# Kernel tuning notes

Measured on AMD Instinct MI355X. Metric: run time of the kernel, lower is better.

Reference implementation:

```python
import jax, jax.numpy as jnp
import numpy as np
from jax import lax

B, L = 4, 2048
D_MODEL, D_STATE, D_CONV, EXPAND = 1024, 16, 4, 2
D_INNER = EXPAND * D_MODEL          # 2048
DT_RANK = (D_MODEL + 15) // 16      # 64 (mamba_ssm 'auto')
EPS = 1e-5


def setup_inputs() -> dict:
    key = jax.random.key(0)
    ks = jax.random.split(key, 10)
    s = 0.02
    x = jax.random.normal(ks[0], (B, L, D_MODEL), dtype=jnp.float32)
    ln_w = jnp.ones((D_MODEL,), jnp.float32)
    ln_b = jnp.zeros((D_MODEL,), jnp.float32)
    W_in = jax.random.normal(ks[1], (2 * D_INNER, D_MODEL), jnp.float32) * s
    conv_w = jax.random.normal(ks[2], (D_INNER, 1, D_CONV), jnp.float32) * s
    conv_b = jnp.zeros((D_INNER,), jnp.float32)
    W_x = jax.random.normal(ks[3], (DT_RANK + 2 * D_STATE, D_INNER), jnp.float32) * s
    W_dt = jax.random.normal(ks[4], (D_INNER, DT_RANK), jnp.float32) * s
    b_dt = jax.random.uniform(ks[5], (D_INNER,), jnp.float32, -4.0, -2.0)  # softplus(b)~small dt
    A_log = jnp.log(jnp.tile(jnp.arange(1.0, D_STATE + 1.0, dtype=jnp.float32), (D_INNER, 1)))
    Dp = jnp.ones((D_INNER,), jnp.float32)
    W_out = jax.random.normal(ks[6], (D_MODEL, D_INNER), jnp.float32) * s
    return dict(x=x, ln_w=ln_w, ln_b=ln_b, W_in=W_in, conv_w=conv_w, conv_b=conv_b,
                W_x=W_x, W_dt=W_dt, b_dt=b_dt, A_log=A_log, Dp=Dp, W_out=W_out)


def _mamba_forward(x, ln_w, ln_b, W_in, conv_w, conv_b, W_x, W_dt, b_dt, A_log, Dp, W_out):
    # LayerNorm
    mu = jnp.mean(x, axis=-1, keepdims=True)
    var = jnp.mean(jnp.square(x - mu), axis=-1, keepdims=True)
    xn = (x - mu) * lax.rsqrt(var + EPS) * ln_w + ln_b

    # in_proj -> (x_in, z), each [B, L, D_INNER]
    xz = jnp.einsum('bld,ed->ble', xn, W_in)
    x_in, z = jnp.split(xz, 2, axis=-1)

    # depthwise causal conv1d over time + SiLU
    xt = jnp.transpose(x_in, (0, 2, 1))  # [B, D_INNER, L]
    xc = lax.conv_general_dilated(xt, conv_w, window_strides=(1,),
                                  padding=[(D_CONV - 1, 0)],
                                  feature_group_count=D_INNER)
    xc = jax.nn.silu(jnp.transpose(xc + conv_b[None, :, None], (0, 2, 1)))  # [B, L, D_INNER]

    # SSM parameterization
    x_dbl = jnp.einsum('bld,ed->ble', xc, W_x)  # [B, L, DT_RANK + 2*D_STATE]
    dt_r, Bs, Cs = jnp.split(x_dbl, [DT_RANK, DT_RANK + D_STATE], axis=-1)
    dt = jax.nn.softplus(jnp.einsum('blr,dr->bld', dt_r, W_dt) + b_dt)  # [B, L, D_INNER]
    A = -jnp.exp(A_log)  # [D_INNER, D_STATE]

    # selective scan over time (time-major)
    def step(h, inp):
        dt_t, B_t, C_t, u_t = inp  # [B,dI], [B,dS], [B,dS], [B,dI]
        dA = jnp.exp(dt_t[:, :, None] * A)                     # [B, dI, dS]
        h = dA * h + (dt_t * u_t)[:, :, None] * B_t[:, None, :]
        y = jnp.sum(h * C_t[:, None, :], axis=-1)              # [B, dI]
        return h, y

    h0 = jnp.zeros((B, D_INNER, D_STATE), x.dtype)
    xs = (jnp.swapaxes(dt, 0, 1), jnp.swapaxes(Bs, 0, 1),
          jnp.swapaxes(Cs, 0, 1), jnp.swapaxes(xc, 0, 1))
    _, ys = lax.scan(step, h0, xs)
    y = jnp.swapaxes(ys, 0, 1) + xc * Dp  # [B, L, D_INNER]

    # gate + out_proj + residual
    y = y * jax.nn.silu(z)
    out = jnp.einsum('ble,de->bld', y, W_out)
    return x + out


def reference(x, ln_w, ln_b, W_in, conv_w, conv_b, W_x, W_dt, b_dt, A_log, Dp, W_out):
    return _mamba_forward(x, ln_w, ln_b, W_in, conv_w, conv_b, W_x, W_dt, b_dt, A_log, Dp, W_out)
```

## Files before the change

kernel.cpp:

```cpp
#include <hip/hip_runtime.h>
#include <math.h>

#define BB 4
#define LL 2048
#define DM 1024
#define DI 2048
#define DS 16
#define DTR 64
#define TCH 256
#define TT 16

typedef unsigned short bf16;
typedef __attribute__((ext_vector_type(8))) short bf16x8;
typedef __attribute__((ext_vector_type(4))) float f32x4;

__device__ inline float b2f(bf16 u) { return __uint_as_float(((unsigned)u) << 16); }
__device__ inline bf16 f2b(float f) {
    unsigned u = __float_as_uint(f);
    u += 0x7FFF + ((u >> 16) & 1);
    return (bf16)(u >> 16);
}

__device__ inline float4 ld4(const float* p) { return *(const float4*)p; }
__device__ inline float4 ld4(const bf16* p) {
    ushort4 v = *(const ushort4*)p;
    return make_float4(b2f(v.x), b2f(v.y), b2f(v.z), b2f(v.w));
}
__device__ inline void st1(float* p, float v) { *p = v; }
__device__ inline void st1(bf16* p, float v) { *p = f2b(v); }

__device__ inline float softplus_fast(float v) {
    return (v > 15.f) ? v : __logf(1.f + __expf(v));
}

__device__ inline void gld_lds16(const void* g, void* l) {
    __builtin_amdgcn_global_load_lds(
        (const __attribute__((address_space(1))) unsigned int*)g,
        (__attribute__((address_space(3))) unsigned int*)l, 16, 0, 0);
}

__global__ __launch_bounds__(256) void f2b_kernel(const float* __restrict__ in,
    bf16* __restrict__ out, int n4)
{
    int i = blockIdx.x * 256 + threadIdx.x;
    if (i >= n4) return;
    float4 v = *(const float4*)(in + (size_t)i * 4);
    ushort4 o = { f2b(v.x), f2b(v.y), f2b(v.z), f2b(v.w) };
    *(ushort4*)(out + (size_t)i * 4) = o;
}

__global__ __launch_bounds__(256) void convw_transpose(
    const float* __restrict__ cw, bf16* __restrict__ cwt)
{
    int d = blockIdx.x * 256 + threadIdx.x;
    if (d >= DI) return;
    float4 w = *(const float4*)(cw + d * 4);
    cwt[0 * DI + d] = f2b(w.x);
    cwt[1 * DI + d] = f2b(w.y);
    cwt[2 * DI + d] = f2b(w.z);
    cwt[3 * DI + d] = f2b(w.w);
}

__global__ void af_init(int* f) { if (threadIdx.x == 0) *f = 0; }

__global__ __launch_bounds__(256) void af_check(const float* __restrict__ A, int* f)
{
    int g = blockIdx.x * 256 + threadIdx.x;
    int d = g >> 4, s = g & 15;
    float a0 = __expf(A[(size_t)d * DS]);
    float as = __expf(A[g]);
    float tgt = (float)(s + 1) * a0;
    if (fabsf(as - tgt) > 1e-5f * fabsf(tgt) + 1e-30f) atomicOr(f, 1);
}

__global__ __launch_bounds__(256) void ln_kernel(const float* __restrict__ x,
    const float* __restrict__ w, const float* __restrict__ b,
    bf16* __restrict__ xn)
{
    int row = blockIdx.x;
    int tid = threadIdx.x;
    const float* xr = x + (size_t)row * DM;
    float4 v = *(const float4*)(xr + tid * 4);
    float s1 = v.x + v.y + v.z + v.w;
    float s2 = v.x * v.x + v.y * v.y + v.z * v.z + v.w * v.w;
    #pragma unroll
    for (int o = 32; o > 0; o >>= 1) {
        s1 += __shfl_xor(s1, o);
        s2 += __shfl_xor(s2, o);
    }
    __shared__ float r1[4], r2[4];
    __shared__ float smu, srs;
    int wv = tid >> 6;
    if ((tid & 63) == 0) { r1[wv] = s1; r2[wv] = s2; }
    __syncthreads();
    if (tid == 0) {
        float t1 = r1[0] + r1[1] + r1[2] + r1[3];
        float t2 = r2[0] + r2[1] + r2[2] + r2[3];
        float mu = t1 * (1.0f / DM);
        float var = t2 * (1.0f / DM) - mu * mu;
        smu = mu;
        srs = rsqrtf(var + 1e-5f);
    }
    __syncthreads();
    float mu = smu, rs = srs;
    float4 wv4 = *(const float4*)(w + tid * 4);
    float4 bv4 = *(const float4*)(b + tid * 4);
    ushort4 o;
    o.x = f2b((v.x - mu) * rs * wv4.x + bv4.x);
    o.y = f2b((v.y - mu) * rs * wv4.y + bv4.y);
    o.z = f2b((v.z - mu) * rs * wv4.z + bv4.z);
    o.w = f2b((v.w - mu) * rs * wv4.w + bv4.w);
    *(ushort4*)(xn + (size_t)row * DM + tid * 4) = o;
}

#define BARR  do { asm volatile("" ::: "memory"); __builtin_amdgcn_s_barrier(); \
                   asm volatile("" ::: "memory"); } while (0)
#define LGKM0 do { asm volatile("s_waitcnt lgkmcnt(0)" ::: "memory"); \
                   __builtin_amdgcn_sched_barrier(0); } while (0)
#define VMC4  asm volatile("s_waitcnt vmcnt(4)" ::: "memory")

template<int EPI, typename TC>
__global__ __launch_bounds__(512, 2) void gemm_8p(
    const bf16* __restrict__ A, int lda,
    const bf16* __restrict__ B, int ldb,
    TC* __restrict__ C, int ldc,
    int K, const float* __restrict__ aux, int nbn)
{
    __shared__ bf16 lds[65536];
    char* L = (char*)lds;
    const int tid = threadIdx.x;
    const int lane = tid & 63;
    const int w = tid >> 6;
    const int wm = w >> 2;
    const int wn = w & 3;

    int nwg = gridDim.x;
    int bid = blockIdx.x;
    int sb = bid;
    if ((nwg & 7) == 0) sb = (bid & 7) * (nwg >> 3) + (bid >> 3);
    const int m0 = (sb / nbn) * 256;
    const int n0 = (sb % nbn) * 256;

    const size_t lda2 = (size_t)lda * 2;
    const size_t ldb2 = (size_t)ldb * 2;
    const int l8 = lane >> 3;
    const int scol = ((lane & 7) ^ l8) << 4;
    const size_t offA = (size_t)(w * 8 + l8) * lda2 + scol;
    const size_t offB = (size_t)(w * 8 + l8) * ldb2 + scol;
    const char* Ab = (const char*)A + (size_t)m0 * lda2;
    const char* Bb = (const char*)B + (size_t)n0 * ldb2;

    const int fm = lane & 15, fq = lane >> 4;
    const int prow = fm * 128;
    const int px0 = (fq << 4) ^ ((fm & 7) << 4);
    const int px1 = (64 | (fq << 4)) ^ ((fm & 7) << 4);
    const char* Lar = L + wm * 16384 + prow;
    const char* Lbr = L + 65536 + (wn >> 1) * 16384 + (wn & 1) * 8192 + prow;

    f32x4 acc[8][4] = {};
    bf16x8 a_[2][2], b_[4][2];

#define ST_A(sbuf, hh, t) do { \
    const char* s_ = Ab + (size_t)(hh) * 128 * lda2 + (size_t)(t) * 128 + offA; \
    gld_lds16(s_,             L + (sbuf) * 32768 + (hh) * 16384 + w * 1024); \
    gld_lds16(s_ + 64 * lda2, L + (sbuf) * 32768 + (hh) * 16384 + 8192 + w * 1024); \
  } while (0)
#define ST_B(sbuf, hh, t) do { \
    const char* s_ = Bb + (size_t)(hh) * 128 * ldb2 + (size_t)(t) * 128 + offB; \
    gld_lds16(s_,             L + 65536 + (sbuf) * 32768 + (hh) * 16384 + w * 1024); \
    gld_lds16(s_ + 64 * ldb2, L + 65536 + (sbuf) * 32768 + (hh) * 16384 + 8192 + w * 1024); \
  } while (0)
#define DS_A(rb, q) do { \
    a_[0][0] = *(const bf16x8*)(Lar + (rb) * 32768 + ((q) * 32 +  0) * 128 + px0); \
    a_[0][1] = *(const bf16x8*)(Lar + (rb) * 32768 + ((q) * 32 +  0) * 128 + px1); \
    a_[1][0] = *(const bf16x8*)(Lar + (rb) * 32768 + ((q) * 32 + 16) * 128 + px0); \
    a_[1][1] = *(const bf16x8*)(Lar + (rb) * 32768 + ((q) * 32 + 16) * 128 + px1); \
  } while (0)
#define DS_B(rb) do { \
    _Pragma("unroll") \
    for (int ni = 0; ni < 4; ni++) { \
      b_[ni][0] = *(const bf16x8*)(Lbr + (rb) * 32768 + ni * 2048 + px0); \
      b_[ni][1] = *(const bf16x8*)(Lbr + (rb) * 32768 + ni * 2048 + px1); \
    } } while (0)
#define MFMA_Q(q) do { \
    __builtin_amdgcn_s_setprio(1); \
    _Pragma("unroll") \
    for (int mi = 0; mi < 2; mi++) \
      _Pragma("unroll") \
      for (int ni = 0; ni < 4; ni++) { \
        acc[(q)*2+mi][ni] = __builtin_amdgcn_mfma_f32_16x16x32_bf16( \
            a_[mi][0], b_[ni][0], acc[(q)*2+mi][ni], 0, 0, 0); \
        acc[(q)*2+mi][ni] = __builtin_amdgcn_mfma_f32_16x16x32_bf16( \
            a_[mi][1], b_[ni][1], acc[(q)*2+mi][ni], 0, 0, 0); \
      } \
    __builtin_amdgcn_s_setprio(0); \
  } while (0)

    const int NT = K >> 6;
    ST_B(0, 0, 0); ST_B(0, 1, 0);
    ST_A(0, 0, 0); ST_A(0, 1, 0);
    ST_B(1, 0, 1); ST_B(1, 1, 1);
    VMC4;
    BARR;

    for (int t0 = 0; t0 < NT; t0 += 2) {
        const int tA1 = t0 + 1;
        const int tN2 = (t0 + 2 < NT) ? t0 + 2 : NT - 1;
        const int tN3 = (t0 + 3 < NT) ? t0 + 3 : NT - 1;
        DS_A(0, 0); DS_B(0); ST_A(1, 0, tA1);
        BARR; LGKM0; MFMA_Q(0); BARR;
        DS_A(0, 1); ST_A(1, 1, tA1);
        BARR; LGKM0; MFMA_Q(1); BARR;
        DS_A(0, 2); ST_B(0, 0, tN2);
        BARR; LGKM0; MFMA_Q(2); BARR;
        DS_A(0, 3); ST_B(0, 1, tN2);
        VMC4;
        BARR; LGKM0; MFMA_Q(3); BARR;
        DS_A(1, 0); DS_B(1); ST_A(0, 0, tN2);
        BARR; LGKM0; MFMA_Q(0); BARR;
        DS_A(1, 1); ST_A(0, 1, tN2);
        BARR; LGKM0; MFMA_Q(1); BARR;
        DS_A(1, 2); ST_B(1, 0, tN3);
        BARR; LGKM0; MFMA_Q(2); BARR;
        DS_A(1, 3); ST_B(1, 1, tN3);
        VMC4;
        BARR; LGKM0; MFMA_Q(3); BARR;
    }
    asm volatile("s_waitcnt vmcnt(0)" ::: "memory");

    #pragma unroll
    for (int i = 0; i < 8; i++) {
        #pragma unroll
        for (int ni = 0; ni < 4; ni++) {
            int n = n0 + wn * 64 + ni * 16 + fm;
            #pragma unroll
            for (int r = 0; r < 4; r++) {
                int m = m0 + wm * 128 + i * 16 + fq * 4 + r;
                float v = acc[i][ni][r];
                if (EPI == 2) v += aux[(size_t)m * ldc + n];
                st1(&C[(size_t)m * ldc + n], v);
            }
        }
    }
#undef ST_A
#undef ST_B
#undef DS_A
#undef DS_B
#undef MFMA_Q
}

template<int EPI, typename TC>
__global__ __launch_bounds__(256) void gemm_mfma(
    const bf16* __restrict__ A, int lda,
    const bf16* __restrict__ B, int ldb,
    TC* __restrict__ C, int ldc,
    int K, const float* __restrict__ aux)
{
    __shared__ bf16 As[128 * 32];
    __shared__ bf16 Bs[128 * 32];
    const int tid = threadIdx.x;
    const int lane = tid & 63;
    const int w = tid >> 6;
    const int wm = w >> 1, wn = w & 1;
    const int m0 = blockIdx.y * 128, n0 = blockIdx.x * 128;

    const int srow = lane >> 2;
    const int schunk = (lane & 3) * 8;

    const int fm = lane & 15;
    const int fq = lane >> 4;

    f32x4 acc[4][4] = {};

    for (int kt = 0; kt < K; kt += 32) {
        #pragma unroll
        for (int i = 0; i < 2; i++) {
            int r0 = i * 64 + w * 16;
            gld_lds16(A + (size_t)(m0 + r0 + srow) * lda + kt + schunk, &As[r0 * 32]);
            gld_lds16(B + (size_t)(n0 + r0 + srow) * ldb + kt + schunk, &Bs[r0 * 32]);
        }
        __syncthreads();
        bf16x8 af[4], bfr[4];
        #pragma unroll
        for (int i = 0; i < 4; i++) {
            af[i]  = *(const bf16x8*)&As[(wm * 64 + i * 16 + fm) * 32 + fq * 8];
            bfr[i] = *(const bf16x8*)&Bs[(wn * 64 + i * 16 + fm) * 32 + fq * 8];
        }
        #pragma unroll
        for (int i = 0; i < 4; i++)
            #pragma unroll
            for (int j = 0; j < 4; j++)
                acc[i][j] = __builtin_amdgcn_mfma_f32_16x16x32_bf16(
                    af[i], bfr[j], acc[i][j], 0, 0, 0);
        __syncthreads();
    }

    #pragma unroll
    for (int i = 0; i < 4; i++) {
        #pragma unroll
        for (int r = 0; r < 4; r++) {
            int m = m0 + wm * 64 + i * 16 + fq * 4 + r;
            #pragma unroll
            for (int j = 0; j < 4; j++) {
                int n = n0 + wn * 64 + j * 16 + fm;
                float v = acc[i][j][r];
                if (EPI == 1) {
                    v = softplus_fast(v + aux[n]);
                } else if (EPI == 2) {
                    v += aux[(size_t)m * ldc + n];
                }
                st1(&C[(size_t)m * ldc + n], v);
            }
        }
    }
}

__global__ __launch_bounds__(256) void xproj_mfma(
    const bf16* __restrict__ A,
    const bf16* __restrict__ Bm,
    float* __restrict__ Cx,
    bf16* __restrict__ dtr)
{
    __shared__ bf16 As[32 * 32];
    __shared__ bf16 Bs[128 * 32];
    const int tid = threadIdx.x;
    const int lane = tid & 63;
    const int w = tid >> 6;
    const int wm = w >> 1, wn = w & 1;
    const int m0 = blockIdx.x * 32;
    const int srow = lane >> 2;
    const int schunk = (lane & 3) * 8;
    const int fm = lane & 15;
    const int fq = lane >> 4;
    f32x4 acc[3] = {};
    for (int kt = 0; kt < DI; kt += 32) {
        if (w < 2) {
            int r0 = w * 16;
            gld_lds16(A + (size_t)(m0 + r0 + srow) * DI + kt + schunk, &As[r0 * 32]);
        }
        {
            int r0 = w * 32;
            gld_lds16(Bm + (size_t)(r0 + srow) * DI + kt + schunk, &Bs[r0 * 32]);
            gld_lds16(Bm + (size_t)(r0 + 16 + srow) * DI + kt + schunk, &Bs[(r0 + 16) * 32]);
        }
        __syncthreads();
        bf16x8 af = *(const bf16x8*)&As[(wm * 16 + fm) * 32 + fq * 8];
        #pragma unroll
        for (int j = 0; j < 3; j++) {
            bf16x8 bf = *(const bf16x8*)&Bs[((wn * 3 + j) * 16 + fm) * 32 + fq * 8];
            acc[j] = __builtin_amdgcn_mfma_f32_16x16x32_bf16(af, bf, acc[j], 0, 0, 0);
        }
        __syncthreads();
    }
    #pragma unroll
    for (int j = 0; j < 3; j++) {
        int col = (wn * 3 + j) * 16 + fm;
        #pragma unroll
        for (int r = 0; r < 4; r++) {
            int m = m0 + wm * 16 + fq * 4 + r;
            float v = acc[j][r];
            Cx[(size_t)m * 96 + col] = v;
            if (col < 64) dtr[(size_t)m * 64 + col] = f2b(v);
        }
    }
}

template<int EPI, typename TA, typename TB, typename TC>
__global__ __launch_bounds__(256) void gemm_nt(
    const TA* __restrict__ A, int lda,
    const TB* __restrict__ B, int ldb,
    TC* __restrict__ C, int ldc,
    int M, int N, int K,
    const float* __restrict__ aux)
{
    __shared__ float As[16][64];
    __shared__ float Bs[16][64];
    int tid = threadIdx.x;
    int m0 = blockIdx.y * 64, n0 = blockIdx.x * 64;
    int lr = tid >> 2;
    int lc = (tid & 3) * 4;
    int tm = tid >> 4;
    int tn = tid & 15;
    float acc[4][4] = {};
    for (int kt = 0; kt < K; kt += 16) {
        float4 av = ld4(A + (size_t)(m0 + lr) * lda + kt + lc);
        float4 bv = make_float4(0.f, 0.f, 0.f, 0.f);
        if (n0 + lr < N)
            bv = ld4(B + (size_t)(n0 + lr) * ldb + kt + lc);
        As[lc + 0][lr] = av.x; As[lc + 1][lr] = av.y;
        As[lc + 2][lr] = av.z; As[lc + 3][lr] = av.w;
        Bs[lc + 0][lr] = bv.x; Bs[lc + 1][lr] = bv.y;
        Bs[lc + 2][lr] = bv.z; Bs[lc + 3][lr] = bv.w;
        __syncthreads();
        #pragma unroll
        for (int k = 0; k < 16; k++) {
            float4 a4 = *(const float4*)&As[k][tm * 4];
            float4 b4 = *(const float4*)&Bs[k][tn * 4];
            float am[4] = {a4.x, a4.y, a4.z, a4.w};
            float bn[4] = {b4.x, b4.y, b4.z, b4.w};
            #pragma unroll
            for (int i = 0; i < 4; i++)
                #pragma unroll
                for (int j = 0; j < 4; j++)
                    acc[i][j] = fmaf(am[i], bn[j], acc[i][j]);
        }
        __syncthreads();
    }
    #pragma unroll
    for (int i = 0; i < 4; i++) {
        int m = m0 + tm * 4 + i;
        #pragma unroll
        for (int j = 0; j < 4; j++) {
            int n = n0 + tn * 4 + j;
            if (n >= N) continue;
            float v = acc[i][j];
            if (EPI == 1) {
                v = softplus_fast(v + aux[n]);
            }
            st1(&C[(size_t)m * ldc + n], v);
        }
    }
}

__global__ __launch_bounds__(256) void conv_silu_kernel(
    const bf16* __restrict__ xz, const bf16* __restrict__ cwt,
    const float* __restrict__ cb, bf16* __restrict__ xc)
{
    int idx = blockIdx.x * 256 + threadIdx.x;
    int d8 = idx & (DI / 8 - 1);
    int bl = idx >> 8;
    int l = bl & (LL - 1);
    int d0 = d8 * 8;
    float4 b0 = *(const float4*)(cb + d0);
    float4 b1 = *(const float4*)(cb + d0 + 4);
    float acc[8] = {b0.x, b0.y, b0.z, b0.w, b1.x, b1.y, b1.z, b1.w};
    #pragma unroll
    for (int k = 0; k < 4; k++) {
        if (l - 3 + k < 0) continue;
        bf16x8 xv = *(const bf16x8*)(xz + (size_t)(bl - 3 + k) * (2 * DI) + d0);
        bf16x8 wv = *(const bf16x8*)(cwt + k * DI + d0);
        #pragma unroll
        for (int j = 0; j < 8; j++)
            acc[j] = fmaf(b2f((bf16)xv[j]), b2f((bf16)wv[j]), acc[j]);
    }
    bf16x8 o;
    #pragma unroll
    for (int j = 0; j < 8; j++)
        o[j] = (short)f2b(acc[j] / (1.f + __expf(-acc[j])));
    *(bf16x8*)(xc + (size_t)bl * DI + d0) = o;
}

template<int NCC>
__global__ __launch_bounds__(256) void scan_part1(
    const float* __restrict__ xdbl, const bf16* __restrict__ dty,
    const bf16* __restrict__ xc, const float* __restrict__ A_log,
    float* __restrict__ P, float* __restrict__ S, const int* __restrict__ aflag)
{
    __shared__ bf16 sdt[TT][TCH];
    __shared__ bf16 su[TT][TCH];
    __shared__ alignas(16) float sBC[TT][32];
    const int CH = LL / NCC;
    int bid = blockIdx.x;
    int cg = bid & 7;
    int c  = (bid >> 3) & (NCC - 1);
    int b  = (bid >> 3) / NCC;
    int d0 = cg * TCH;
    int tid = threadIdx.x;
    int w = tid >> 6, l = tid & 63;
    int lrow = l >> 5, lcol = (l & 31) * 8;
    int brow = l >> 3, bcol = (l & 7) * 4;
    int d = d0 + tid;

    const int structured = (__builtin_amdgcn_readfirstlane(aflag[0]) == 0);

    float Ads[16];
    #pragma unroll
    for (int q = 0; q < 4; q++) {
        float4 a4 = *(const float4*)&A_log[(size_t)d * DS + q * 4];
        Ads[q*4+0] = -__expf(a4.x); Ads[q*4+1] = -__expf(a4.y);
        Ads[q*4+2] = -__expf(a4.z); Ads[q*4+3] = -__expf(a4.w);
    }
    const float A0 = Ads[0];
    float h[16];
    #pragma unroll
    for (int s = 0; s < 16; s++) h[s] = 0.f;
    float dsum = 0.f;

    const size_t rowbase = (size_t)b * LL + c * CH;
    for (int t0 = 0; t0 < CH; t0 += TT) {
        #pragma unroll
        for (int pp = 0; pp < 2; pp++) {
            int r0 = (pp * 4 + w) * 2;
            size_t grow = rowbase + t0 + r0 + lrow;
            gld_lds16(dty + grow * DI + d0 + lcol, &sdt[r0][0]);
            gld_lds16(xc  + grow * DI + d0 + lcol, &su[r0][0]);
        }
        if (w < 2)
            gld_lds16(xdbl + (rowbase + t0 + w * 8 + brow) * 96 + DTR + bcol,
                      &sBC[w * 8][0]);
        __syncthreads();
        for (int t = 0; t < TT; t++) {
            float dtv = b2f(sdt[t][tid]);
            float uv  = b2f(su[t][tid]);
            float tmp = dtv * uv;
            dsum += dtv;
            const float4* bc = (const float4*)&sBC[t][0];
            float4 B0 = bc[0], B1 = bc[1], B2 = bc[2], B3 = bc[3];
            float Bv[16] = {B0.x,B0.y,B0.z,B0.w, B1.x,B1.y,B1.z,B1.w,
                            B2.x,B2.y,B2.z,B2.w, B3.x,B3.y,B3.z,B3.w};
            if (structured) {
                float e1 = __expf(dtv * A0);
                float dA = e1;
                #pragma unroll
                for (int s = 0; s < 16; s++) {
                    h[s] = dA * h[s] + tmp * Bv[s];
                    dA *= e1;
                }
            } else {
                #pragma unroll
                for (int s = 0; s < 16; s++) {
                    float dA = __expf(dtv * Ads[s]);
                    h[s] = dA * h[s] + tmp * Bv[s];
                }
            }
        }
        __syncthreads();
    }
    size_t o = ((size_t)(b * NCC + c) * DI + d) * DS;
    #pragma unroll
    for (int q = 0; q < 4; q++) {
        float4 pv = make_float4(__expf(Ads[q*4+0]*dsum), __expf(Ads[q*4+1]*dsum),
                                __expf(Ads[q*4+2]*dsum), __expf(Ads[q*4+3]*dsum));
        *(float4*)&P[o + q*4] = pv;
        *(float4*)&S[o + q*4] = make_float4(h[q*4], h[q*4+1], h[q*4+2], h[q*4+3]);
    }
}

template<int NCC>
__global__ __launch_bounds__(256) void scan_combine(
    const float* __restrict__ P, float* __restrict__ S)
{
    int g = blockIdx.x * 256 + threadIdx.x;
    int b = g >> 15;
    int rem = g & 32767;
    float h = 0.f;
    #pragma unroll
    for (int c = 0; c < NCC; c++) {
        size_t o = ((size_t)(b * NCC + c) << 15) + rem;
        float p = P[o], sv = S[o];
        S[o] = h;
        h = p * h + sv;
    }
}

template<int NCC>
__global__ __launch_bounds__(256) void scan_part2(
    const float* __restrict__ xdbl, bf16* __restrict__ dty,
    const bf16* __restrict__ xc, const bf16* __restrict__ xz,
    const float* __restrict__ A_log, const float* __restrict__ Dp,
    const float* __restrict__ Hin, const int* __restrict__ aflag)
{
    __shared__ bf16 sdt[TT][TCH];
    __shared__ bf16 su[TT][TCH];
    __shared__ bf16 sz[TT][TCH];
    __shared__ alignas(16) float sBC[TT][32];
    const int CH = LL / NCC;
    int bid = blockIdx.x;
    int cg = bid & 7;
    int c  = (bid >> 3) & (NCC - 1);
    int b  = (bid >> 3) / NCC;
    int d0 = cg * TCH;
    int tid = threadIdx.x;
    int w = tid >> 6, l = tid & 63;
    int lrow = l >> 5, lcol = (l & 31) * 8;
    int brow = l >> 3, bcol = (l & 7) * 4;
    int d = d0 + tid;

    const int structured = (__builtin_amdgcn_readfirstlane(aflag[0]) == 0);

    float Ads[16];
    #pragma unroll
    for (int q = 0; q < 4; q++) {
        float4 a4 = *(const float4*)&A_log[(size_t)d * DS + q * 4];
        Ads[q*4+0] = -__expf(a4.x); Ads[q*4+1] = -__expf(a4.y);
        Ads[q*4+2] = -__expf(a4.z); Ads[q*4+3] = -__expf(a4.w);
    }
    const float A0 = Ads[0];
    float h[16];
    size_t ho = ((size_t)(b * NCC + c) * DI + d) * DS;
    #pragma unroll
    for (int q = 0; q < 4; q++) {
        float4 hv = *(const float4*)&Hin[ho + q*4];
        h[q*4] = hv.x; h[q*4+1] = hv.y; h[q*4+2] = hv.z; h[q*4+3] = hv.w;
    }
    float dpd = Dp[d];

    const size_t rowbase = (size_t)b * LL + c * CH;
    for (int t0 = 0; t0 < CH; t0 += TT) {
        #pragma unroll
        for (int pp = 0; pp < 2; pp++) {
            int r0 = (pp * 4 + w) * 2;
            size_t grow = rowbase + t0 + r0 + lrow;
            gld_lds16(dty + grow * DI + d0 + lcol, &sdt[r0][0]);
            gld_lds16(xc  + grow * DI + d0 + lcol, &su[r0][0]);
            gld_lds16(xz  + grow * (2 * DI) + DI + d0 + lcol, &sz[r0][0]);
        }
        if (w < 2)
            gld_lds16(xdbl + (rowbase + t0 + w * 8 + brow) * 96 + DTR + bcol,
                      &sBC[w * 8][0]);
        __syncthreads();
        for (int t = 0; t < TT; t++) {
            float dtv = b2f(sdt[t][tid]);
            float uv  = b2f(su[t][tid]);
            float tmp = dtv * uv;
            const float4* bc = (const float4*)&sBC[t][0];
            float4 B0 = bc[0], B1 = bc[1], B2 = bc[2], B3 = bc[3];
            float4 C0 = bc[4], C1 = bc[5], C2 = bc[6], C3 = bc[7];
            float Bv[16] = {B0.x,B0.y,B0.z,B0.w, B1.x,B1.y,B1.z,B1.w,
                            B2.x,B2.y,B2.z,B2.w, B3.x,B3.y,B3.z,B3.w};
            float Cv[16] = {C0.x,C0.y,C0.z,C0.w, C1.x,C1.y,C1.z,C1.w,
                            C2.x,C2.y,C2.z,C2.w, C3.x,C3.y,C3.z,C3.w};
            float y0 = 0.f, y1 = 0.f;
            if (structured) {
                float e1 = __expf(dtv * A0);
                float dA = e1;
                #pragma unroll
                for (int s = 0; s < 16; s++) {
                    h[s] = dA * h[s] + tmp * Bv[s];
                    if (s & 1) y1 = fmaf(h[s], Cv[s], y1);
                    else       y0 = fmaf(h[s], Cv[s], y0);
                    dA *= e1;
                }
            } else {
                #pragma unroll
                for (int s = 0; s < 16; s++) {
                    float dA = __expf(dtv * Ads[s]);
                    h[s] = dA * h[s] + tmp * Bv[s];
                    if (s & 1) y1 = fmaf(h[s], Cv[s], y1);
                    else       y0 = fmaf(h[s], Cv[s], y0);
                }
            }
            float y = y0 + y1;
            float zv = b2f(sz[t][tid]);
            float yo = (y + uv * dpd) * (zv / (1.f + __expf(-zv)));
            dty[(rowbase + t0 + t) * DI + d] = f2b(yo);
        }
        __syncthreads();
    }
}

__global__ __launch_bounds__(256) void scan_mono(
    const float* __restrict__ xdbl, bf16* __restrict__ dty,
    const bf16* __restrict__ xc, const bf16* __restrict__ xz,
    const float* __restrict__ A_log, const float* __restrict__ Dp)
{
    const int TC = 64;
    int b = blockIdx.x >> 7;
    int dblk = blockIdx.x & 127;
    int d0 = dblk * 16;
    int tid = threadIdx.x;
    int s = tid & 15;
    int dg = tid >> 4;
    int d = d0 + dg;
    float Ads = -__expf(A_log[(size_t)d * DS + s]);
    float h = 0.f;
    __shared__ float sdt[TC][16], su[TC][16], sB[TC][16], sC[TC][16], sy[TC][16];
    const size_t rowbase = (size_t)b * LL;
    int wi = tid >> 2;
    int wj = (tid & 3) * 4;
    float4 dpv = *(const float4*)(Dp + d0 + wj);
    for (int t0 = 0; t0 < LL; t0 += TC) {
        {
            size_t g = (rowbase + t0 + wi) * (size_t)DI + d0 + wj;
            *(float4*)&sdt[wi][wj] = ld4(dty + g);
            *(float4*)&su[wi][wj]  = ld4(xc + g);
        }
        #pragma unroll
        for (int r = 0; r < 4; r++) {
            int i = (tid >> 4) + r * 16;
            size_t g = (rowbase + t0 + i) * 96;
            sB[i][s] = xdbl[g + DTR + s];
            sC[i][s] = xdbl[g + DTR + DS + s];
        }
        __syncthreads();
        for (int i = 0; i < TC; i++) {
            float dtv = sdt[i][dg];
            float dA = __expf(dtv * Ads);
            h = dA * h + dtv * su[i][dg] * sB[i][s];
            float yp = h * sC[i][s];
            yp += __shfl_xor(yp, 1);
            yp += __shfl_xor(yp, 2);
            yp += __shfl_xor(yp, 4);
            yp += __shfl_xor(yp, 8);
            if (s == 0) sy[i][dg] = yp;
        }
        __syncthreads();
        {
            size_t g  = (rowbase + t0 + wi) * (size_t)DI + d0 + wj;
            size_t gz = (rowbase + t0 + wi) * (size_t)(2 * DI) + DI + d0 + wj;
            float4 zv = ld4(xz + gz);
            float4 yv = *(const float4*)&sy[wi][wj];
            float4 uv = *(const float4*)&su[wi][wj];
            ushort4 o;
            o.x = f2b((yv.x + uv.x * dpv.x) * (zv.x / (1.f + __expf(-zv.x))));
            o.y = f2b((yv.y + uv.y * dpv.y) * (zv.y / (1.f + __expf(-zv.y))));
            o.z = f2b((yv.z + uv.z * dpv.z) * (zv.z / (1.f + __expf(-zv.z))));
            o.w = f2b((yv.w + uv.w * dpv.w) * (zv.w / (1.f + __expf(-zv.w))));
            *(ushort4*)(dty + g) = o;
        }
        __syncthreads();
    }
}

__global__ __launch_bounds__(256) void conv_silu_slow(
    const bf16* __restrict__ xz, const float* __restrict__ cw,
    const float* __restrict__ cb, bf16* __restrict__ xc)
{
    int idx = blockIdx.x * 256 + threadIdx.x;
    int d4 = idx & (DI / 4 - 1);
    int bl = idx >> 9;
    int l = bl & (LL - 1);
    int d0 = d4 * 4;
    float4 bias = *(const float4*)(cb + d0);
    float acc[4] = {bias.x, bias.y, bias.z, bias.w};
    #pragma unroll
    for (int k = 0; k < 4; k++) {
        if (l - 3 + k < 0) continue;
        float4 xv = ld4(xz + (size_t)(bl - 3 + k) * (2 * DI) + d0);
        acc[0] = fmaf(xv.x, cw[(d0 + 0) * 4 + k], acc[0]);
        acc[1] = fmaf(xv.y, cw[(d0 + 1) * 4 + k], acc[1]);
        acc[2] = fmaf(xv.z, cw[(d0 + 2) * 4 + k], acc[2]);
        acc[3] = fmaf(xv.w, cw[(d0 + 3) * 4 + k], acc[3]);
    }
    ushort4 o;
    o.x = f2b(acc[0] / (1.f + __expf(-acc[0])));
    o.y = f2b(acc[1] / (1.f + __expf(-acc[1])));
    o.z = f2b(acc[2] / (1.f + __expf(-acc[2])));
    o.w = f2b(acc[3] / (1.f + __expf(-acc[3])));
    *(ushort4*)(xc + (size_t)bl * DI + d0) = o;
}

extern "C" void kernel_launch(void* const* d_in, const int* in_sizes, int n_in,
                              void* d_out, int out_size, void* d_ws, size_t ws_size,
                              hipStream_t stream)
{
    const float* x      = (const float*)d_in[0];
    const float* ln_w   = (const float*)d_in[1];
    const float* ln_b   = (const float*)d_in[2];
    const float* W_in   = (const float*)d_in[3];
    const float* conv_w = (const float*)d_in[4];
    const float* conv_b = (const float*)d_in[5];
    const float* W_x    = (const float*)d_in[6];
    const float* W_dt   = (const float*)d_in[7];
    const float* b_dt   = (const float*)d_in[8];
    const float* A_log  = (const float*)d_in[9];
    const float* Dp     = (const float*)d_in[10];
    const float* W_out  = (const float*)d_in[11];
    float* out = (float*)d_out;

    const size_t R = (size_t)BB * LL;

    bf16*  xz    = (bf16*)d_ws;
    bf16*  dty   = xz + R * 2 * DI;
    float* xdbl  = (float*)(dty + R * DI);
    float* Pbuf  = xdbl + R * 96;

    const size_t headB = (size_t)((char*)Pbuf - (char*)d_ws);
    const size_t tailB = (size_t)(128 * DI + DI * DTR + R * DTR + 4 * DI) * 2 + 64;
    const size_t ps32B = (size_t)BB * 32 * DI * DS * 4;
    const size_t ps16B = (size_t)BB * 16 * DI * DS * 4;
    const int ncc = (ws_size >= headB + 2 * ps32B + tailB) ? 32 : 16;
    const size_t psB = (ncc == 32) ? ps32B : ps16B;

    float* Sbuf   = (float*)((char*)Pbuf + psB);
    bf16*  W_x_b  = (bf16*)((char*)Sbuf + psB);
    bf16*  W_dt_b = W_x_b + 128 * DI;
    bf16*  dtr    = W_dt_b + DI * DTR;
    bf16*  cwt    = dtr + R * DTR;
    int*   aflag  = (int*)(cwt + 4 * DI);
    const size_t ws_need = (size_t)((char*)(aflag + 16) - (char*)d_ws);
    const bool fast = ws_size >= ws_need;

    bf16*  W_in_b  = dty;
    bf16*  W_out_b = xz;

    bf16* xn = (bf16*)d_out;
    bf16* xc = (bf16*)d_out;

    f2b_kernel<<<(2 * DI * DM / 4) / 256, 256, 0, stream>>>(W_in, W_in_b, 2 * DI * DM / 4);
    if (fast) {
        f2b_kernel<<<(96 * DI / 4 + 255) / 256, 256, 0, stream>>>(W_x, W_x_b, 96 * DI / 4);
        f2b_kernel<<<(DI * DTR / 4 + 255) / 256, 256, 0, stream>>>(W_dt, W_dt_b, DI * DTR / 4);
        convw_transpose<<<DI / 256, 256, 0, stream>>>(conv_w, cwt);
        af_init<<<1, 64, 0, stream>>>(aflag);
        af_check<<<DI * DS / 256, 256, 0, stream>>>(A_log, aflag);
    }

    ln_kernel<<<(int)R, 256, 0, stream>>>(x, ln_w, ln_b, xn);

    gemm_8p<0, bf16><<<dim3((int)(R / 256) * (2 * DI / 256)), 512, 0, stream>>>(
        xn, DM, W_in_b, DM, xz, 2 * DI, DM, nullptr, 2 * DI / 256);

    if (fast) {
        conv_silu_kernel<<<(int)(R * DI / 8 / 256), 256, 0, stream>>>(
            xz, cwt, conv_b, xc);
        xproj_mfma<<<(int)(R / 32), 256, 0, stream>>>(xc, W_x_b, xdbl, dtr);
        gemm_mfma<1, bf16><<<dim3(DI / 128, R / 128), 256, 0, stream>>>(
            dtr, DTR, W_dt_b, DTR, dty, DI, DTR, b_dt);
        if (ncc == 32) {
            scan_part1<32><<<BB * 32 * (DI / TCH), 256, 0, stream>>>(
                xdbl, dty, xc, A_log, Pbuf, Sbuf, aflag);
            scan_combine<32><<<BB * DI * DS / 256, 256, 0, stream>>>(Pbuf, Sbuf);
            scan_part2<32><<<BB * 32 * (DI / TCH), 256, 0, stream>>>(
                xdbl, dty, xc, xz, A_log, Dp, Sbuf, aflag);
        } else {
            scan_part1<16><<<BB * 16 * (DI / TCH), 256, 0, stream>>>(
                xdbl, dty, xc, A_log, Pbuf, Sbuf, aflag);
            scan_combine<16><<<BB * DI * DS / 256, 256, 0, stream>>>(Pbuf, Sbuf);
            scan_part2<16><<<BB * 16 * (DI / TCH), 256, 0, stream>>>(
                xdbl, dty, xc, xz, A_log, Dp, Sbuf, aflag);
        }
    } else {
        conv_silu_slow<<<(int)(R * DI / 4 / 256), 256, 0, stream>>>(
            xz, conv_w, conv_b, xc);
        gemm_nt<0><<<dim3(2, R / 64), 256, 0, stream>>>(
            xc, DI, W_x, DI, xdbl, 96, (int)R, 96, DI, nullptr);
        gemm_nt<1><<<dim3(DI / 64, R / 64), 256, 0, stream>>>(
            xdbl, 96, W_dt, DTR, dty, DI, (int)R, DI, DTR, b_dt);
        scan_mono<<<BB * (DI / 16), 256, 0, stream>>>(
            xdbl, dty, xc, xz, A_log, Dp);
    }

    f2b_kernel<<<(DM * DI / 4) / 256, 256, 0, stream>>>(W_out, W_out_b, DM * DI / 4);

    gemm_8p<2, float><<<dim3((int)(R / 256) * (DM / 256)), 512, 0, stream>>>(
        dty, DI, W_out_b, DI, out, DM, DI, x, DM / 256);
}
```

Measured before the change: 431.7 us.

## Software-pipeline LDS fragment reads with MFMA in the 8-phase GEMM

Splits each MFMA quarter into two k-halves. The LDS fragment loads for the next quarter (and next buffer's B fragments at quarter 3) are issued between and after those halves, so they overlap matrix work instead of stalling ahead of it. A prologue preloads the first fragments before the loop. This is meant to hide LDS read latency in the GEMM's main loop. It costs extra register pressure from live prefetched fragments, and it relies on barrier and waitcnt placement staying correct under the new read ordering.

```diff
diff --git a/kernel.cpp b/kernel.cpp
--- a/kernel.cpp
+++ b/kernel.cpp
@@ -118,6 +118,7 @@
 #define LGKM0 do { asm volatile("s_waitcnt lgkmcnt(0)" ::: "memory"); \
                    __builtin_amdgcn_sched_barrier(0); } while (0)
 #define VMC4  asm volatile("s_waitcnt vmcnt(4)" ::: "memory")
+#define SCHED0 __builtin_amdgcn_sched_barrier(0)
 
 template<int EPI, typename TC>
 __global__ __launch_bounds__(512, 2) void gemm_8p(
@@ -170,30 +171,39 @@
     gld_lds16(s_,             L + 65536 + (sbuf) * 32768 + (hh) * 16384 + w * 1024); \
     gld_lds16(s_ + 64 * ldb2, L + 65536 + (sbuf) * 32768 + (hh) * 16384 + 8192 + w * 1024); \
   } while (0)
-#define DS_A(rb, q) do { \
-    a_[0][0] = *(const bf16x8*)(Lar + (rb) * 32768 + ((q) * 32 +  0) * 128 + px0); \
-    a_[0][1] = *(const bf16x8*)(Lar + (rb) * 32768 + ((q) * 32 +  0) * 128 + px1); \
-    a_[1][0] = *(const bf16x8*)(Lar + (rb) * 32768 + ((q) * 32 + 16) * 128 + px0); \
-    a_[1][1] = *(const bf16x8*)(Lar + (rb) * 32768 + ((q) * 32 + 16) * 128 + px1); \
+#define DS_A1(rb, q, kh) do { \
+    a_[0][kh] = *(const bf16x8*)(Lar + (rb) * 32768 + ((q) * 32 +  0) * 128 + ((kh) ? px1 : px0)); \
+    a_[1][kh] = *(const bf16x8*)(Lar + (rb) * 32768 + ((q) * 32 + 16) * 128 + ((kh) ? px1 : px0)); \
   } while (0)
-#define DS_B(rb) do { \
+#define DS_Bh(rb, kh) do { \
     _Pragma("unroll") \
-    for (int ni = 0; ni < 4; ni++) { \
-      b_[ni][0] = *(const bf16x8*)(Lbr + (rb) * 32768 + ni * 2048 + px0); \
-      b_[ni][1] = *(const bf16x8*)(Lbr + (rb) * 32768 + ni * 2048 + px1); \
-    } } while (0)
-#define MFMA_Q(q) do { \
-    __builtin_amdgcn_s_setprio(1); \
+    for (int ni = 0; ni < 4; ni++) \
+      b_[ni][kh] = *(const bf16x8*)(Lbr + (rb) * 32768 + ni * 2048 + ((kh) ? px1 : px0)); \
+  } while (0)
+#define MFMA_H(q, kh) do { \
     _Pragma("unroll") \
     for (int mi = 0; mi < 2; mi++) \
       _Pragma("unroll") \
-      for (int ni = 0; ni < 4; ni++) { \
+      for (int ni = 0; ni < 4; ni++) \
         acc[(q)*2+mi][ni] = __builtin_amdgcn_mfma_f32_16x16x32_bf16( \
-            a_[mi][0], b_[ni][0], acc[(q)*2+mi][ni], 0, 0, 0); \
-        acc[(q)*2+mi][ni] = __builtin_amdgcn_mfma_f32_16x16x32_bf16( \
-            a_[mi][1], b_[ni][1], acc[(q)*2+mi][ni], 0, 0, 0); \
-      } \
+            a_[mi][kh], b_[ni][kh], acc[(q)*2+mi][ni], 0, 0, 0); \
+  } while (0)
+#define PHASE(rb, q, rb2, q2, STAGE, DOVMC) do { \
+    STAGE; \
+    if (DOVMC) VMC4; \
+    BARR; LGKM0; \
+    __builtin_amdgcn_s_setprio(1); \
+    MFMA_H(q, 0); \
     __builtin_amdgcn_s_setprio(0); \
+    DS_A1(rb2, q2, 0); \
+    if ((q) == 3) DS_Bh(rb2, 0); \
+    SCHED0; \
+    __builtin_amdgcn_s_setprio(1); \
+    MFMA_H(q, 1); \
+    __builtin_amdgcn_s_setprio(0); \
+    DS_A1(rb2, q2, 1); \
+    if ((q) == 3) DS_Bh(rb2, 1); \
+    BARR; \
   } while (0)
 
     const int NT = K >> 6;
@@ -202,29 +212,21 @@
     ST_B(1, 0, 1); ST_B(1, 1, 1);
     VMC4;
     BARR;
+    DS_Bh(0, 0); DS_Bh(0, 1);
+    DS_A1(0, 0, 0); DS_A1(0, 0, 1);
 
     for (int t0 = 0; t0 < NT; t0 += 2) {
         const int tA1 = t0 + 1;
         const int tN2 = (t0 + 2 < NT) ? t0 + 2 : NT - 1;
         const int tN3 = (t0 + 3 < NT) ? t0 + 3 : NT - 1;
-        DS_A(0, 0); DS_B(0); ST_A(1, 0, tA1);
-        BARR; LGKM0; MFMA_Q(0); BARR;
-        DS_A(0, 1); ST_A(1, 1, tA1);
-        BARR; LGKM0; MFMA_Q(1); BARR;
-        DS_A(0, 2); ST_B(0, 0, tN2);
-        BARR; LGKM0; MFMA_Q(2); BARR;
-        DS_A(0, 3); ST_B(0, 1, tN2);
-        VMC4;
-        BARR; LGKM0; MFMA_Q(3); BARR;
-        DS_A(1, 0); DS_B(1); ST_A(0, 0, tN2);
-        BARR; LGKM0; MFMA_Q(0); BARR;
-        DS_A(1, 1); ST_A(0, 1, tN2);
-        BARR; LGKM0; MFMA_Q(1); BARR;
-        DS_A(1, 2); ST_B(1, 0, tN3);
-        BARR; LGKM0; MFMA_Q(2); BARR;
-        DS_A(1, 3); ST_B(1, 1, tN3);
-        VMC4;
-        BARR; LGKM0; MFMA_Q(3); BARR;
+        PHASE(0, 0, 0, 1, ST_A(1, 0, tA1), 0);
+        PHASE(0, 1, 0, 2, ST_A(1, 1, tA1), 0);
+        PHASE(0, 2, 0, 3, ST_B(0, 0, tN2), 0);
+        PHASE(0, 3, 1, 0, ST_B(0, 1, tN2), 1);
+        PHASE(1, 0, 1, 1, ST_A(0, 0, tN2), 0);
+        PHASE(1, 1, 1, 2, ST_A(0, 1, tN2), 0);
+        PHASE(1, 2, 1, 3, ST_B(1, 0, tN3), 0);
+        PHASE(1, 3, 0, 0, ST_B(1, 1, tN3), 1);
     }
     asm volatile("s_waitcnt vmcnt(0)" ::: "memory");
 
@@ -244,9 +246,10 @@
     }
 #undef ST_A
 #undef ST_B
-#undef DS_A
-#undef DS_B
-#undef MFMA_Q
+#undef DS_A1
+#undef DS_Bh
+#undef MFMA_H
+#undef PHASE
 }
 
 template<int EPI, typename TC>
```

After: 448.3 us. +3.9%, slower.
